# Performance work log

Measured on AMD Instinct MI355X. Metric: run time of the kernel, lower is better.

## Reference

```python
import jax, jax.numpy as jnp
import numpy as np

N_DATA = 12288
N_QUERY = 12288
DIM = 3
RADIUS = 0.085  # gives ~32 neighbors/query for uniform points in [0,1]^3


def setup_inputs() -> dict:
    key = jax.random.key(0)
    k1, k2 = jax.random.split(key)
    data = jax.random.uniform(k1, (N_DATA, DIM), dtype=jnp.float32)
    queries = jax.random.uniform(k2, (N_QUERY, DIM), dtype=jnp.float32)
    radius = jnp.float32(RADIUS)
    return {"data": data, "queries": queries, "radius": radius}


def reference(data, queries, radius):
    # Dense, jit-compatible equivalent of KDTree.query_radius with return_distance=True.
    # Original returns ragged CSR (neighbors_index, neighbors_row_splits, weights=dists**2).
    # Fixed-shape encoding: boolean membership mask [M, N] (row m, col n True iff
    # data[n] is a neighbor of queries[m]; CSR indices = nonzero cols in row order),
    # row_splits [M+1] (exact CSR splits), and dense weights [M, N] = squared
    # distance where within radius else 0 (CSR weights = masked entries in row order).
    sq_d = jnp.sum(data * data, axis=-1)          # [N]
    sq_q = jnp.sum(queries * queries, axis=-1)    # [M]
    # ||q - d||^2 = ||q||^2 + ||d||^2 - 2 q.d  (GEMM form)
    d2 = sq_q[:, None] + sq_d[None, :] - 2.0 * (queries @ data.T)  # [M, N]
    d2 = jnp.maximum(d2, 0.0)
    mask = d2 <= radius * radius                  # [M, N]
    counts = jnp.sum(mask, axis=-1, dtype=jnp.int32)  # [M]
    row_splits = jnp.concatenate(
        [jnp.zeros((1,), jnp.int32), jnp.cumsum(counts)]
    )  # [M+1], matches nbr_dict['neighbors_row_splits']
    weights = jnp.where(mask, d2, 0.0)            # dists**2, masked
    return row_splits, mask, weights
```

## Files before the change

kernel.cpp:

```cpp
#include <hip/hip_runtime.h>


#define TILE 2048

__global__ __launch_bounds__(256) void nbr_kernel(
    const float* __restrict__ data,
    const float* __restrict__ queries,
    const float* __restrict__ radius_p,
    float* __restrict__ out,
    int* __restrict__ counts,
    int N, long long mask_off, long long w_off)
{
    __shared__ float tile[TILE * 3];

    const int m = blockIdx.x;
    const int tid = threadIdx.x;

    const float r = radius_p[0];
    const float r2 = __fmul_rn(r, r);
    const float q0 = queries[3 * m + 0];
    const float q1 = queries[3 * m + 1];
    const float q2 = queries[3 * m + 2];
    const float sq_q = __fadd_rn(
        __fadd_rn(__fmul_rn(q0, q0), __fmul_rn(q1, q1)), __fmul_rn(q2, q2));

    float* mask_row = out + mask_off + (long long)m * N;
    float* w_row    = out + w_off    + (long long)m * N;

    int cnt = 0;

    auto compute = [&](float d0, float d1, float d2e, float& mv, float& wv) -> int {
        const float sq_d = __fadd_rn(
            __fadd_rn(__fmul_rn(d0, d0), __fmul_rn(d1, d1)), __fmul_rn(d2e, d2e));
        const float dot = __fmaf_rn(q2, d2e, __fmaf_rn(q1, d1, __fmul_rn(q0, d0)));
        const float s = __fadd_rn(sq_q, sq_d);
        float v = __fsub_rn(s, __fmul_rn(2.0f, dot));
        v = fmaxf(v, 0.0f);
        const bool in = (v <= r2);
        mv = in ? 1.0f : 0.0f;
        wv = in ? v : 0.0f;
        return in ? 1 : 0;
    };

    for (int tb = 0; tb < N; tb += TILE) {
        const int lim = min(TILE, N - tb);

        __syncthreads();
        if (lim == TILE) {
            const float4* src = reinterpret_cast<const float4*>(data + 3LL * tb);
            float4* dst = reinterpret_cast<float4*>(tile);
            #pragma unroll
            for (int w = 0; w < TILE * 3 / 4 / 256; ++w)
                dst[w * 256 + tid] = src[w * 256 + tid];
        } else {
            for (int w = tid; w < lim * 3; w += 256)
                tile[w] = data[3LL * tb + w];
        }
        __syncthreads();

        if (lim == TILE) {
            #pragma unroll
            for (int k = 0; k < TILE / 256; ++k) {
                const int e = k * 256 + tid;
                const float d0  = tile[3 * e + 0];
                const float d1  = tile[3 * e + 1];
                const float d2e = tile[3 * e + 2];
                float mv, wv;
                cnt += compute(d0, d1, d2e, mv, wv);
                mask_row[tb + e] = mv;
                w_row[tb + e] = wv;
            }
        } else {
            for (int e = tid; e < lim; e += 256) {
                const float d0  = tile[3 * e + 0];
                const float d1  = tile[3 * e + 1];
                const float d2e = tile[3 * e + 2];
                float mv, wv;
                cnt += compute(d0, d1, d2e, mv, wv);
                mask_row[tb + e] = mv;
                w_row[tb + e] = wv;
            }
        }
    }

    for (int off = 32; off > 0; off >>= 1) cnt += __shfl_down(cnt, off);
    __shared__ int lds_cnt;
    if (tid == 0) lds_cnt = 0;
    __syncthreads();
    if ((tid & 63) == 0) atomicAdd(&lds_cnt, cnt);
    __syncthreads();
    if (tid == 0) counts[m] = lds_cnt;
}

__global__ __launch_bounds__(256) void scan_kernel(
    const int* __restrict__ counts, float* __restrict__ out, int M)
{
    __shared__ int sums[256];
    const int t = threadIdx.x;
    const int CH = (M + 255) / 256;
    const int base = t * CH;

    int local[64];
    int s = 0;
    for (int i = 0; i < CH; ++i) {
        const int v = (base + i < M) ? counts[base + i] : 0;
        local[i] = v;
        s += v;
    }
    sums[t] = s;
    __syncthreads();
    for (int off = 1; off < 256; off <<= 1) {
        const int v = (t >= off) ? sums[t - off] : 0;
        __syncthreads();
        sums[t] += v;
        __syncthreads();
    }
    int prefix = sums[t] - s;
    for (int i = 0; i < CH; ++i) {
        if (base + i < M) out[base + i] = (float)prefix;
        prefix += local[i];
    }
    if (t == 255) out[M] = (float)prefix;
}

extern "C" void kernel_launch(void* const* d_in, const int* in_sizes, int n_in,
                              void* d_out, int out_size, void* d_ws, size_t ws_size,
                              hipStream_t stream) {
    const float* data    = (const float*)d_in[0];
    const float* queries = (const float*)d_in[1];
    const float* radius  = (const float*)d_in[2];

    const int N = in_sizes[0] / 3;
    const int M = in_sizes[1] / 3;

    float* out = (float*)d_out;
    int* counts = (int*)d_ws;

    const long long mask_off = (long long)M + 1;
    const long long w_off = mask_off + (long long)M * N;

    nbr_kernel<<<M, 256, 0, stream>>>(data, queries, radius, out, counts,
                                      N, mask_off, w_off);
    scan_kernel<<<1, 256, 0, stream>>>(counts, out, M);
}
```

Baseline: 1.245 ms.

## Process eight query rows per block with aligned float4 output stores

Each block now handles eight query rows, reusing the staged data tile across them and computing squared data norms once per point. Columns are regrouped so that row stores become 16-byte aligned float4 writes, with the first three and trailing columns handled separately. This aims to raise store efficiency on the bandwidth-heavy mask and weight outputs and cut redundant tile loads. It costs more registers per thread and fewer blocks, and it assumes M is divisible by eight.

```diff
diff --git a/kernel.cpp b/kernel.cpp
--- a/kernel.cpp
+++ b/kernel.cpp
@@ -1,9 +1,12 @@
 #include <hip/hip_runtime.h>
 
 
-#define TILE 2048
+#define BLK 256
+#define ROWS 8
+#define GTILE 512
+#define TWORDS (GTILE * 12)
 
-__global__ __launch_bounds__(256) void nbr_kernel(
+__global__ __launch_bounds__(BLK) void nbr_kernel(
     const float* __restrict__ data,
     const float* __restrict__ queries,
     const float* __restrict__ radius_p,
@@ -11,85 +14,135 @@
     int* __restrict__ counts,
     int N, long long mask_off, long long w_off)
 {
-    __shared__ float tile[TILE * 3];
+    __shared__ float4 tile4[GTILE * 3];
+    float* tile = reinterpret_cast<float*>(tile4);
+    __shared__ int lds_cnt[ROWS];
 
-    const int m = blockIdx.x;
     const int tid = threadIdx.x;
+    const int m0 = blockIdx.x * ROWS;
 
     const float r = radius_p[0];
     const float r2 = __fmul_rn(r, r);
-    const float q0 = queries[3 * m + 0];
-    const float q1 = queries[3 * m + 1];
-    const float q2 = queries[3 * m + 2];
-    const float sq_q = __fadd_rn(
-        __fadd_rn(__fmul_rn(q0, q0), __fmul_rn(q1, q1)), __fmul_rn(q2, q2));
 
-    float* mask_row = out + mask_off + (long long)m * N;
-    float* w_row    = out + w_off    + (long long)m * N;
+    float q0[ROWS], q1[ROWS], q2[ROWS], sqq[ROWS];
+#pragma unroll
+    for (int rr = 0; rr < ROWS; ++rr) {
+        q0[rr] = queries[3 * (m0 + rr) + 0];
+        q1[rr] = queries[3 * (m0 + rr) + 1];
+        q2[rr] = queries[3 * (m0 + rr) + 2];
+        sqq[rr] = __fadd_rn(__fadd_rn(__fmul_rn(q0[rr], q0[rr]),
+                                      __fmul_rn(q1[rr], q1[rr])),
+                            __fmul_rn(q2[rr], q2[rr]));
+    }
 
-    int cnt = 0;
+    float* mrow[ROWS];
+    float* wrow[ROWS];
+#pragma unroll
+    for (int rr = 0; rr < ROWS; ++rr) {
+        mrow[rr] = out + mask_off + (long long)(m0 + rr) * N;
+        wrow[rr] = out + w_off    + (long long)(m0 + rr) * N;
+    }
 
-    auto compute = [&](float d0, float d1, float d2e, float& mv, float& wv) -> int {
-        const float sq_d = __fadd_rn(
-            __fadd_rn(__fmul_rn(d0, d0), __fmul_rn(d1, d1)), __fmul_rn(d2e, d2e));
-        const float dot = __fmaf_rn(q2, d2e, __fmaf_rn(q1, d1, __fmul_rn(q0, d0)));
-        const float s = __fadd_rn(sq_q, sq_d);
-        float v = __fsub_rn(s, __fmul_rn(2.0f, dot));
-        v = fmaxf(v, 0.0f);
-        const bool in = (v <= r2);
-        mv = in ? 1.0f : 0.0f;
-        wv = in ? v : 0.0f;
-        return in ? 1 : 0;
-    };
+    int cnt[ROWS];
+#pragma unroll
+    for (int rr = 0; rr < ROWS; ++rr) cnt[rr] = 0;
 
-    for (int tb = 0; tb < N; tb += TILE) {
-        const int lim = min(TILE, N - tb);
+    const int ng = (N - 3) / 4;
+    const int nspec = N - 4 * ng;
+
+    if (tid < nspec) {
+        const int c = (tid < 3) ? tid : (4 * ng + tid);
+        const float d0  = data[3 * c + 0];
+        const float d1  = data[3 * c + 1];
+        const float d2e = data[3 * c + 2];
+        const float sqd = __fadd_rn(
+            __fadd_rn(__fmul_rn(d0, d0), __fmul_rn(d1, d1)),
+            __fmul_rn(d2e, d2e));
+#pragma unroll
+        for (int rr = 0; rr < ROWS; ++rr) {
+            const float dot = __fmaf_rn(q2[rr], d2e,
+                                __fmaf_rn(q1[rr], d1, __fmul_rn(q0[rr], d0)));
+            float v = __fsub_rn(__fadd_rn(sqq[rr], sqd), __fmul_rn(2.0f, dot));
+            v = fmaxf(v, 0.0f);
+            const bool in = (v <= r2);
+            mrow[rr][c] = in ? 1.0f : 0.0f;
+            wrow[rr][c] = in ? v : 0.0f;
+            cnt[rr] += in ? 1 : 0;
+        }
+    }
+
+    for (int g0 = 0; g0 < ng; g0 += GTILE) {
+        const int ngt = min(GTILE, ng - g0);
+        const long long W0 = 3LL * (3 + 4LL * (long long)g0);
+        const int lim = 12 * ngt;
 
         __syncthreads();
-        if (lim == TILE) {
-            const float4* src = reinterpret_cast<const float4*>(data + 3LL * tb);
-            float4* dst = reinterpret_cast<float4*>(tile);
-            #pragma unroll
-            for (int w = 0; w < TILE * 3 / 4 / 256; ++w)
-                dst[w * 256 + tid] = src[w * 256 + tid];
+        if (lim == TWORDS) {
+#pragma unroll
+            for (int k = 0; k < TWORDS / BLK; ++k)
+                tile[k * BLK + tid] = data[W0 + k * BLK + tid];
         } else {
-            for (int w = tid; w < lim * 3; w += 256)
-                tile[w] = data[3LL * tb + w];
+            for (int w = tid; w < lim; w += BLK)
+                tile[w] = data[W0 + w];
         }
         __syncthreads();
 
-        if (lim == TILE) {
-            #pragma unroll
-            for (int k = 0; k < TILE / 256; ++k) {
-                const int e = k * 256 + tid;
-                const float d0  = tile[3 * e + 0];
-                const float d1  = tile[3 * e + 1];
-                const float d2e = tile[3 * e + 2];
-                float mv, wv;
-                cnt += compute(d0, d1, d2e, mv, wv);
-                mask_row[tb + e] = mv;
-                w_row[tb + e] = wv;
-            }
-        } else {
-            for (int e = tid; e < lim; e += 256) {
-                const float d0  = tile[3 * e + 0];
-                const float d1  = tile[3 * e + 1];
-                const float d2e = tile[3 * e + 2];
-                float mv, wv;
-                cnt += compute(d0, d1, d2e, mv, wv);
-                mask_row[tb + e] = mv;
-                w_row[tb + e] = wv;
+#pragma unroll
+        for (int k = 0; k < GTILE / BLK; ++k) {
+            const int sl = k * BLK + tid;
+            if (sl < ngt) {
+                const float4 A = tile4[3 * sl + 0];
+                const float4 B = tile4[3 * sl + 1];
+                const float4 C = tile4[3 * sl + 2];
+                const float d0[4]  = {A.x, A.w, B.z, C.y};
+                const float d1[4]  = {A.y, B.x, B.w, C.z};
+                const float d2e[4] = {A.z, B.y, C.x, C.w};
+                float sqd[4];
+#pragma unroll
+                for (int j = 0; j < 4; ++j)
+                    sqd[j] = __fadd_rn(
+                        __fadd_rn(__fmul_rn(d0[j], d0[j]),
+                                  __fmul_rn(d1[j], d1[j])),
+                        __fmul_rn(d2e[j], d2e[j]));
+
+                const int c = 3 + 4 * (g0 + sl);
+#pragma unroll
+                for (int rr = 0; rr < ROWS; ++rr) {
+                    float mv[4], wv[4];
+                    int cc = 0;
+#pragma unroll
+                    for (int j = 0; j < 4; ++j) {
+                        const float dot = __fmaf_rn(q2[rr], d2e[j],
+                                            __fmaf_rn(q1[rr], d1[j],
+                                              __fmul_rn(q0[rr], d0[j])));
+                        float v = __fsub_rn(__fadd_rn(sqq[rr], sqd[j]),
+                                            __fmul_rn(2.0f, dot));
+                        v = fmaxf(v, 0.0f);
+                        const bool in = (v <= r2);
+                        mv[j] = in ? 1.0f : 0.0f;
+                        wv[j] = in ? v : 0.0f;
+                        cc += in ? 1 : 0;
+                    }
+                    cnt[rr] += cc;
+                    *reinterpret_cast<float4*>(mrow[rr] + c) =
+                        make_float4(mv[0], mv[1], mv[2], mv[3]);
+                    *reinterpret_cast<float4*>(wrow[rr] + c) =
+                        make_float4(wv[0], wv[1], wv[2], wv[3]);
+                }
             }
         }
     }
 
-    for (int off = 32; off > 0; off >>= 1) cnt += __shfl_down(cnt, off);
-    __shared__ int lds_cnt;
-    if (tid == 0) lds_cnt = 0;
+    if (tid < ROWS) lds_cnt[tid] = 0;
     __syncthreads();
-    if ((tid & 63) == 0) atomicAdd(&lds_cnt, cnt);
+#pragma unroll
+    for (int rr = 0; rr < ROWS; ++rr) {
+        int c = cnt[rr];
+        for (int off = 32; off > 0; off >>= 1) c += __shfl_down(c, off);
+        if ((tid & 63) == 0) atomicAdd(&lds_cnt[rr], c);
+    }
     __syncthreads();
-    if (tid == 0) counts[m] = lds_cnt;
+    if (tid < ROWS) counts[m0 + tid] = lds_cnt[tid];
 }
 
 __global__ __launch_bounds__(256) void scan_kernel(
@@ -139,7 +192,7 @@
     const long long mask_off = (long long)M + 1;
     const long long w_off = mask_off + (long long)M * N;
 
-    nbr_kernel<<<M, 256, 0, stream>>>(data, queries, radius, out, counts,
-                                      N, mask_off, w_off);
+    nbr_kernel<<<M / ROWS, BLK, 0, stream>>>(data, queries, radius, out, counts,
+                                             N, mask_off, w_off);
     scan_kernel<<<1, 256, 0, stream>>>(counts, out, M);
 }
```

After: 1.276 ms. +2.5%, slower.

## Tile by column windows with per-thread register-resident data points across many query rows

Applied to the files above, without the earlier changes.

The kernel now assigns each block a 1024-column data window, loaded once into LDS and then into registers, four points per thread. The block then loops over a strided set of query rows, so data loads and squared-norm work are reused across queries instead of reloaded for every query. Each thread writes four contiguous floats per row. Row counts are accumulated with shared-memory atomics and then global atomics, which needs an extra zeroing kernel. The code assumes N is a multiple of 1024 and that M divides evenly by the row-group count, so it has no tail handling.

```diff
diff --git a/kernel.cpp b/kernel.cpp
--- a/kernel.cpp
+++ b/kernel.cpp
@@ -1,95 +1,94 @@
 #include <hip/hip_runtime.h>
 
 
-#define TILE 2048
+#define BLK 256
+#define COLW 1024
+#define MAXITERS 128
 
-__global__ __launch_bounds__(256) void nbr_kernel(
+__global__ __launch_bounds__(BLK) void zero_counts(int* __restrict__ counts,
+                                                   int M) {
+    const int i = blockIdx.x * BLK + threadIdx.x;
+    if (i < M) counts[i] = 0;
+}
+
+__global__ __launch_bounds__(BLK) void nbr_kernel(
     const float* __restrict__ data,
     const float* __restrict__ queries,
     const float* __restrict__ radius_p,
     float* __restrict__ out,
     int* __restrict__ counts,
-    int N, long long mask_off, long long w_off)
+    int N, int WINDOWS, int RGR, int ITERS,
+    long long mask_off, long long w_off)
 {
-    __shared__ float tile[TILE * 3];
+    __shared__ float tile[COLW * 3];
+    __shared__ int rowcnt[MAXITERS];
 
-    const int m = blockIdx.x;
     const int tid = threadIdx.x;
+    const int w  = blockIdx.x % WINDOWS;
+    const int rg = blockIdx.x / WINDOWS;
+    const long long colbase = (long long)w * COLW;
+
+    {
+        const float4* src =
+            reinterpret_cast<const float4*>(data + 3 * colbase);
+        float4* dst = reinterpret_cast<float4*>(tile);
+#pragma unroll
+        for (int i = 0; i < COLW * 3 / 4 / BLK; ++i)
+            dst[i * BLK + tid] = src[i * BLK + tid];
+    }
+    for (int i = tid; i < ITERS; i += BLK) rowcnt[i] = 0;
+    __syncthreads();
+
+    const float4 A = reinterpret_cast<const float4*>(tile)[3 * tid + 0];
+    const float4 B = reinterpret_cast<const float4*>(tile)[3 * tid + 1];
+    const float4 C = reinterpret_cast<const float4*>(tile)[3 * tid + 2];
+    const float d0[4]  = {A.x, A.w, B.z, C.y};
+    const float d1[4]  = {A.y, B.x, B.w, C.z};
+    const float d2e[4] = {A.z, B.y, C.x, C.w};
+    float sqd[4];
+#pragma unroll
+    for (int j = 0; j < 4; ++j)
+        sqd[j] = __fadd_rn(
+            __fadd_rn(__fmul_rn(d0[j], d0[j]), __fmul_rn(d1[j], d1[j])),
+            __fmul_rn(d2e[j], d2e[j]));
 
     const float r = radius_p[0];
     const float r2 = __fmul_rn(r, r);
-    const float q0 = queries[3 * m + 0];
-    const float q1 = queries[3 * m + 1];
-    const float q2 = queries[3 * m + 2];
-    const float sq_q = __fadd_rn(
-        __fadd_rn(__fmul_rn(q0, q0), __fmul_rn(q1, q1)), __fmul_rn(q2, q2));
 
-    float* mask_row = out + mask_off + (long long)m * N;
-    float* w_row    = out + w_off    + (long long)m * N;
+    const long long c0 = colbase + 4 * tid;
 
-    int cnt = 0;
+    for (int t = 0; t < ITERS; ++t) {
+        const int m = t * RGR + rg;
+        const float q0 = queries[3 * m + 0];
+        const float q1 = queries[3 * m + 1];
+        const float q2 = queries[3 * m + 2];
+        const float sqq = __fadd_rn(
+            __fadd_rn(__fmul_rn(q0, q0), __fmul_rn(q1, q1)),
+            __fmul_rn(q2, q2));
 
-    auto compute = [&](float d0, float d1, float d2e, float& mv, float& wv) -> int {
-        const float sq_d = __fadd_rn(
-            __fadd_rn(__fmul_rn(d0, d0), __fmul_rn(d1, d1)), __fmul_rn(d2e, d2e));
-        const float dot = __fmaf_rn(q2, d2e, __fmaf_rn(q1, d1, __fmul_rn(q0, d0)));
-        const float s = __fadd_rn(sq_q, sq_d);
-        float v = __fsub_rn(s, __fmul_rn(2.0f, dot));
-        v = fmaxf(v, 0.0f);
-        const bool in = (v <= r2);
-        mv = in ? 1.0f : 0.0f;
-        wv = in ? v : 0.0f;
-        return in ? 1 : 0;
-    };
+        float* mrow = out + mask_off + (long long)m * N + c0;
+        float* wrow = out + w_off    + (long long)m * N + c0;
 
-    for (int tb = 0; tb < N; tb += TILE) {
-        const int lim = min(TILE, N - tb);
-
-        __syncthreads();
-        if (lim == TILE) {
-            const float4* src = reinterpret_cast<const float4*>(data + 3LL * tb);
-            float4* dst = reinterpret_cast<float4*>(tile);
-            #pragma unroll
-            for (int w = 0; w < TILE * 3 / 4 / 256; ++w)
-                dst[w * 256 + tid] = src[w * 256 + tid];
-        } else {
-            for (int w = tid; w < lim * 3; w += 256)
-                tile[w] = data[3LL * tb + w];
+        int cc = 0;
+#pragma unroll
+        for (int j = 0; j < 4; ++j) {
+            const float dot = __fmaf_rn(q2, d2e[j],
+                                __fmaf_rn(q1, d1[j], __fmul_rn(q0, d0[j])));
+            float v = __fsub_rn(__fadd_rn(sqq, sqd[j]),
+                                __fmul_rn(2.0f, dot));
+            v = fmaxf(v, 0.0f);
+            const bool in = (v <= r2);
+            mrow[j] = in ? 1.0f : 0.0f;
+            wrow[j] = in ? v : 0.0f;
+            cc += in ? 1 : 0;
         }
-        __syncthreads();
-
-        if (lim == TILE) {
-            #pragma unroll
-            for (int k = 0; k < TILE / 256; ++k) {
-                const int e = k * 256 + tid;
-                const float d0  = tile[3 * e + 0];
-                const float d1  = tile[3 * e + 1];
-                const float d2e = tile[3 * e + 2];
-                float mv, wv;
-                cnt += compute(d0, d1, d2e, mv, wv);
-                mask_row[tb + e] = mv;
-                w_row[tb + e] = wv;
-            }
-        } else {
-            for (int e = tid; e < lim; e += 256) {
-                const float d0  = tile[3 * e + 0];
-                const float d1  = tile[3 * e + 1];
-                const float d2e = tile[3 * e + 2];
-                float mv, wv;
-                cnt += compute(d0, d1, d2e, mv, wv);
-                mask_row[tb + e] = mv;
-                w_row[tb + e] = wv;
-            }
-        }
+        for (int off = 32; off > 0; off >>= 1) cc += __shfl_down(cc, off);
+        if ((tid & 63) == 0) atomicAdd(&rowcnt[t], cc);
     }
 
-    for (int off = 32; off > 0; off >>= 1) cnt += __shfl_down(cnt, off);
-    __shared__ int lds_cnt;
-    if (tid == 0) lds_cnt = 0;
     __syncthreads();
-    if ((tid & 63) == 0) atomicAdd(&lds_cnt, cnt);
-    __syncthreads();
-    if (tid == 0) counts[m] = lds_cnt;
+    for (int t = tid; t < ITERS; t += BLK)
+        atomicAdd(&counts[t * RGR + rg], rowcnt[t]);
 }
 
 __global__ __launch_bounds__(256) void scan_kernel(
@@ -139,7 +138,14 @@
     const long long mask_off = (long long)M + 1;
     const long long w_off = mask_off + (long long)M * N;
 
-    nbr_kernel<<<M, 256, 0, stream>>>(data, queries, radius, out, counts,
-                                      N, mask_off, w_off);
+    const int WINDOWS = N / COLW;
+    int RGR = 128;
+    while ((M % RGR) != 0 || (M / RGR) > MAXITERS) RGR <<= 1;
+    const int ITERS = M / RGR;
+
+    zero_counts<<<(M + BLK - 1) / BLK, BLK, 0, stream>>>(counts, M);
+    nbr_kernel<<<WINDOWS * RGR, BLK, 0, stream>>>(
+        data, queries, radius, out, counts, N, WINDOWS, RGR, ITERS,
+        mask_off, w_off);
     scan_kernel<<<1, 256, 0, stream>>>(counts, out, M);
 }
```

Measured after the change: 1.380 ms. 10.9% more time.
